# Kernel optimization log

Measured on AMD Instinct MI355X. Metric: run time of the kernel, lower is better.

Reference implementation:

```python
import jax, jax.numpy as jnp
import numpy as np

GCN_DIM = 512
POS_EMB_DIM = 64
K = 8
L = 128  # uttr_len
B = 16
PAIR_FEAT = 2 * GCN_DIM + POS_EMB_DIM


def _pair_indices(L, K):
    # Static (trace-time) construction of the windowed pair list, matching the
    # torch masked_select over the full L*L pair grid: row p = i*L + j keeps
    # pairs with |j - i| <= K, in the same row-major order.
    i = np.repeat(np.arange(L), L)
    j = np.tile(np.arange(L), L)
    rel = j - i
    mask = np.abs(rel) <= K
    return i[mask], j[mask], rel[mask]


def setup_inputs() -> dict:
    key = jax.random.key(0)
    k1, k2, k3, k4, k5, k6, k7 = jax.random.split(key, 7)
    h_emo = jax.random.normal(k1, (B, L, GCN_DIM), dtype=jnp.float32)
    h_cause = jax.random.normal(k2, (B, L, GCN_DIM), dtype=jnp.float32)
    # xavier_uniform for embedding table
    lim_e = np.sqrt(6.0 / (2 * K + 1 + POS_EMB_DIM))
    pos_emb = jax.random.uniform(k3, (2 * K + 1, POS_EMB_DIM), minval=-lim_e, maxval=lim_e, dtype=jnp.float32)
    lim1 = np.sqrt(1.0 / PAIR_FEAT)
    W1 = jax.random.uniform(k4, (PAIR_FEAT, PAIR_FEAT), minval=-lim1, maxval=lim1, dtype=jnp.float32)
    b1 = jax.random.uniform(k5, (PAIR_FEAT,), minval=-lim1, maxval=lim1, dtype=jnp.float32)
    W2 = jax.random.uniform(k6, (1, PAIR_FEAT), minval=-lim1, maxval=lim1, dtype=jnp.float32)
    b2 = jax.random.uniform(k7, (1,), minval=-lim1, maxval=lim1, dtype=jnp.float32)
    return {
        "uttr_output_h_emotion": h_emo,
        "uttr_output_h_cause": h_cause,
        "pos_emb": pos_emb,
        "W1": W1,
        "b1": b1,
        "W2": W2,
        "b2": b2,
    }


def reference(uttr_output_h_emotion, uttr_output_h_cause, pos_emb, W1, b1, W2, b2):
    emo_idx, cau_idx, rel_np = _pair_indices(L, K)  # static numpy, length n
    emo_idx_j = jnp.asarray(emo_idx)
    cau_idx_j = jnp.asarray(cau_idx)
    rel = jnp.asarray(rel_np)  # [n], values in [-K, K]

    # windowed pair gather: couples_h = [H_emo[i] ; H_cause[j]]  -> [B, n, 2*g]
    P = jnp.concatenate(
        [uttr_output_h_emotion[:, emo_idx_j, :], uttr_output_h_cause[:, cau_idx_j, :]],
        axis=2,
    )

    # relative-position embedding + Gaussian kernel smoothing (batch-invariant)
    rel_emb = pos_emb[rel + K]  # [n, pos_emb_dim]
    rel_f = rel.astype(jnp.float32)
    kernel = jnp.exp(-jnp.square(rel_f[:, None] - rel_f[None, :]))  # [n, n]
    smoothed = kernel @ rel_emb  # [n, pos_emb_dim]

    couples = jnp.concatenate(
        [P, jnp.broadcast_to(smoothed[None], (P.shape[0],) + smoothed.shape)], axis=2
    )  # [B, n, PAIR_FEAT]

    h = jax.nn.relu(jnp.einsum("bnf,gf->bng", couples, W1) + b1)
    pred = (jnp.einsum("bnf,of->bno", h, W2) + b2).squeeze(-1)  # [B, n]

    emo_cau_pos = jnp.stack([emo_idx_j + 1, cau_idx_j + 1], axis=1)  # [n, 2], int
    return pred, emo_cau_pos
```

## Files before the change

### kernel.cpp

```cpp
#include <hip/hip_runtime.h>

typedef unsigned short u16;
typedef unsigned int u32;
typedef __attribute__((ext_vector_type(4))) float f32x4;
typedef __attribute__((ext_vector_type(8))) __bf16 bf16x8;
typedef __attribute__((ext_vector_type(4))) u16 u16x4;
typedef __attribute__((ext_vector_type(8))) u16 u16x8;
typedef __attribute__((ext_vector_type(4))) float f32x4v;

#define LSEQ 128
#define KW 8
#define NP 2104
#define MTOT 33664
#define FDIM 1088
#define GPAD 1152

#define WS_W1P  0ul
#define WS_EMOB 2506752ul
#define WS_CAUB 4603904ul
#define WS_SB   6701056ul
#define WS_TOFF 6738048ul
#define WS_EC   6738560ul

__device__ __forceinline__ u16 f2bf(float x) {
  union { float f; u32 u; } v; v.f = x;
  u32 r = v.u + 0x7fffu + ((v.u >> 16) & 1u);
  return (u16)(r >> 16);
}

__device__ __forceinline__ float bf2f(u16 x) {
  union { u32 u; float f; } v; v.u = ((u32)x) << 16; return v.f;
}

__device__ __forceinline__ void load_lds16(const void* g, void* l) {
  __builtin_amdgcn_global_load_lds(
      (const __attribute__((address_space(1))) void*)g,
      (__attribute__((address_space(3))) void*)l, 16, 0, 0);
}

__global__ __launch_bounds__(256)
void setup_all(const float* __restrict__ emo, const float* __restrict__ cau,
               const float* __restrict__ pos_emb, const float* __restrict__ W1,
               const float* __restrict__ b1,
               u16* __restrict__ W1p, u16* __restrict__ emoB,
               u16* __restrict__ cauB, u16* __restrict__ Sb,
               int* __restrict__ tab_off, float* __restrict__ out_pos) {
  __shared__ float smL[17 * 64];
  const int bx = blockIdx.x;
  const int t = threadIdx.x;
  if (bx < 612) {
    int idx = bx * 256 + t;
    int g = idx / 136;
    int f = (idx - g * 136) * 8;
    u16x8 o;
    if (g < 1088) {
      f32x4v v0 = *(const f32x4v*)&W1[g * 1088 + f];
      f32x4v v1 = *(const f32x4v*)&W1[g * 1088 + f + 4];
      o[0] = f2bf(v0.x); o[1] = f2bf(v0.y); o[2] = f2bf(v0.z); o[3] = f2bf(v0.w);
      o[4] = f2bf(v1.x); o[5] = f2bf(v1.y); o[6] = f2bf(v1.z); o[7] = f2bf(v1.w);
    } else {
      o = (u16x8)0;
    }
    *(u16x8*)&W1p[(size_t)g * 1088 + f] = o;
  } else if (bx < 1636) {
    int idx = (bx - 612) * 256 + t;
    const float* src;
    u16* dst;
    if (idx < 131072) { src = emo + idx * 8; dst = emoB + idx * 8; }
    else { int k = idx - 131072; src = cau + k * 8; dst = cauB + k * 8; }
    f32x4v v0 = *(const f32x4v*)src;
    f32x4v v1 = *(const f32x4v*)(src + 4);
    u16x8 o;
    o[0] = f2bf(v0.x); o[1] = f2bf(v0.y); o[2] = f2bf(v0.z); o[3] = f2bf(v0.w);
    o[4] = f2bf(v1.x); o[5] = f2bf(v1.y); o[6] = f2bf(v1.z); o[7] = f2bf(v1.w);
    *(u16x8*)dst = o;
  } else if (bx == 1636) {
    if (t < LSEQ) {
      int i = t;
      int off = 0;
      for (int tt = 0; tt < i; ++tt) {
        int lo = tt - KW; if (lo < 0) lo = 0;
        int hi = tt + KW; if (hi > LSEQ - 1) hi = LSEQ - 1;
        off += hi - lo + 1;
      }
      tab_off[i] = off;
      int jlo = i - KW; if (jlo < 0) jlo = 0;
      int jhi = i + KW; if (jhi > LSEQ - 1) jhi = LSEQ - 1;
      for (int j = jlo; j <= jhi; ++j) {
        int p = off + (j - jlo);
        out_pos[2 * p]     = (float)(i + 1);
        out_pos[2 * p + 1] = (float)(j + 1);
      }
    }
  } else {
    for (int idx = t; idx < 17 * 64; idx += 256) {
      int r = idx >> 6, d = idx & 63;
      float acc = 0.f;
      for (int s = 0; s < 17; ++s) {
        float diff = (float)(r - s);
        int a = s - 8; if (a < 0) a = -a;
        float cnt = (float)(128 - a);
        acc += cnt * expf(-diff * diff) * pos_emb[s * 64 + d];
      }
      smL[idx] = acc;
    }
    __syncthreads();
    int idx2 = (bx - 1637) * 256 + t;
    if (idx2 < 17 * 1088) {
      int r = idx2 / 1088;
      int g = idx2 - r * 1088;
      float a = b1[g];
      const float* wr = &W1[(size_t)g * 1088 + 1024];
      const float* sr = &smL[r * 64];
#pragma unroll 8
      for (int d = 0; d < 64; ++d) a = fmaf(sr[d], wr[d], a);
      Sb[r * 1088 + g] = f2bf(a);
    }
  }
}

__global__ __launch_bounds__(256, 4)
void feat_gemm(const u16* __restrict__ emoB, const u16* __restrict__ cauB,
               const u16* __restrict__ W1p, float* __restrict__ EC) {
  __shared__ __align__(16) u16 As2[2][64 * 32];
  __shared__ __align__(16) u16 Bs2[2][128 * 32];

  const int tid = threadIdx.x;
  const int mblk = blockIdx.x;
  const int gbase = blockIdx.y * 128;

  const int lane = tid & 63;
  const int w = tid >> 6;
  const int lrow = lane & 15;
  const int lk = (lane >> 4) * 8;
  const int wm = (w >> 1) * 32;
  const int wn = (w & 1) * 64;

  const int row0 = tid >> 2;
  const int sub = (tid & 3) * 8;

  const u16* Asrc = (mblk < 32) ? emoB : cauB;
  const int arow = (mblk & 31) * 64;
  const int fsel = (mblk < 32) ? 0 : 512;

  const u16* aP = Asrc + (size_t)(arow + row0) * 512 + sub;
  const u16* bP = W1p + (size_t)(gbase + row0) * FDIM + fsel + sub;
  const u16* bQ = bP + 64u * FDIM;

#define FSTAGE(ks, bb)                                                     \
  do {                                                                     \
    const int _f = (ks) * 32;                                              \
    load_lds16(aP + _f, (char*)&As2[bb][0] + tid * 16);                    \
    load_lds16(bP + _f, (char*)&Bs2[bb][0] + tid * 16);                    \
    load_lds16(bQ + _f, (char*)&Bs2[bb][0] + 4096 + tid * 16);             \
  } while (0)

  f32x4 acc[2][4];
#pragma unroll
  for (int mi = 0; mi < 2; ++mi)
#pragma unroll
    for (int ni = 0; ni < 4; ++ni) acc[mi][ni] = (f32x4){0.f, 0.f, 0.f, 0.f};

  FSTAGE(0, 0);
  asm volatile("s_waitcnt vmcnt(0)");
  __builtin_amdgcn_s_barrier();
  __builtin_amdgcn_sched_barrier(0);

  int cur = 0;
#pragma unroll 2
  for (int ks = 0; ks < 16; ++ks) {
    if (ks < 15) FSTAGE(ks + 1, cur ^ 1);

    bf16x8 av[2], bv[4];
#pragma unroll
    for (int mi = 0; mi < 2; ++mi)
      av[mi] = *(const bf16x8*)&As2[cur][(wm + mi * 16 + lrow) * 32 + lk];
#pragma unroll
    for (int ni = 0; ni < 4; ++ni)
      bv[ni] = *(const bf16x8*)&Bs2[cur][(wn + ni * 16 + lrow) * 32 + lk];
#pragma unroll
    for (int mi = 0; mi < 2; ++mi)
#pragma unroll
      for (int ni = 0; ni < 4; ++ni)
        acc[mi][ni] = __builtin_amdgcn_mfma_f32_16x16x32_bf16(av[mi], bv[ni], acc[mi][ni], 0, 0, 0);

    asm volatile("s_waitcnt vmcnt(0)");
    __builtin_amdgcn_s_barrier();
    __builtin_amdgcn_sched_barrier(0);
    cur ^= 1;
  }
#undef FSTAGE

  const int rbase = mblk * 64 + wm + ((lane >> 4) << 2);
#pragma unroll
  for (int mi = 0; mi < 2; ++mi) {
#pragma unroll
    for (int ni = 0; ni < 4; ++ni) {
      const int ocol = gbase + wn + ni * 16 + lrow;
      float* dst = EC + (size_t)(rbase + mi * 16) * GPAD + ocol;
#pragma unroll
      for (int r2 = 0; r2 < 4; ++r2) dst[(size_t)r2 * GPAD] = acc[mi][ni][r2];
    }
  }
}

__global__ __launch_bounds__(256, 4)
void combine(const float* __restrict__ EC, const u16* __restrict__ Sb,
             const float* __restrict__ W2, const float* __restrict__ b2,
             const int* __restrict__ tab_off, float* __restrict__ pred) {
  __shared__ __align__(16) u16 Sl[17 * 1088];
  __shared__ float partA[2][17], partB[2][17];

  const int tid = threadIdx.x;
  const int bid = blockIdx.x;
  const int sb = (bid & 7) * 128 + (bid >> 3);

  {
    char* dst = (char*)&Sl[0];
    const char* src = (const char*)Sb;
#pragma unroll
    for (int it = 0; it < 9; ++it)
      load_lds16(src + it * 4096 + tid * 16, dst + it * 4096 + tid * 16);
    if (tid < 8)
      load_lds16(src + 36864 + tid * 16, dst + 36864 + tid * 16);
  }

  const int w = tid >> 6;
  const int lane = tid & 63;
  const int h = w >> 1;
  const int gh = w & 1;
  const int u = sb * 2 + h;
  const int b = u >> 7;
  const int i = u & 127;
  int jlo = i - KW; if (jlo < 0) jlo = 0;
  int jhi = i + KW; if (jhi > 127) jhi = 127;

  const float bias2 = b2[0];
  const float* Erow = EC + (size_t)(b * 128 + i) * GPAD;
  const float* Cbase = EC + (size_t)(2048 + b * 128) * GPAD;

  const int g0 = gh * 512 + lane * 4;
  const int g1 = g0 + 256;
  const f32x4v e0 = *(const f32x4v*)(Erow + g0);
  const f32x4v e1 = *(const f32x4v*)(Erow + g1);
  const f32x4v w20 = *(const f32x4v*)(W2 + g0);
  const f32x4v w21 = *(const f32x4v*)(W2 + g1);
  float eT = 0.f, w2T = 0.f;
  if (gh) { eT = Erow[1024 + lane]; w2T = W2[1024 + lane]; }

  __syncthreads();

  const float* Crow = Cbase + (size_t)jlo * GPAD;
  f32x4v c0 = *(const f32x4v*)(Crow + g0);
  f32x4v c1 = *(const f32x4v*)(Crow + g1);
  float cT = gh ? Crow[1024 + lane] : 0.f;

  for (int j = jlo; j <= jhi; ++j) {
    f32x4v n0 = c0, n1 = c1; float nT = cT;
    if (j < jhi) {
      const float* Nrow = Cbase + (size_t)(j + 1) * GPAD;
      n0 = *(const f32x4v*)(Nrow + g0);
      n1 = *(const f32x4v*)(Nrow + g1);
      if (gh) nT = Nrow[1024 + lane];
    }
    const int r = j - i + KW;
    const u16* srow = &Sl[r * 1088];
    u16x4 sa = *(const u16x4*)(srow + g0);
    u16x4 sc = *(const u16x4*)(srow + g1);

    float a = 0.f;
    a = fmaf(fmaxf(e0.x + c0.x + bf2f(sa.x), 0.f), w20.x, a);
    a = fmaf(fmaxf(e0.y + c0.y + bf2f(sa.y), 0.f), w20.y, a);
    a = fmaf(fmaxf(e0.z + c0.z + bf2f(sa.z), 0.f), w20.z, a);
    a = fmaf(fmaxf(e0.w + c0.w + bf2f(sa.w), 0.f), w20.w, a);
    a = fmaf(fmaxf(e1.x + c1.x + bf2f(sc.x), 0.f), w21.x, a);
    a = fmaf(fmaxf(e1.y + c1.y + bf2f(sc.y), 0.f), w21.y, a);
    a = fmaf(fmaxf(e1.z + c1.z + bf2f(sc.z), 0.f), w21.z, a);
    a = fmaf(fmaxf(e1.w + c1.w + bf2f(sc.w), 0.f), w21.w, a);
    if (gh) {
      float sT = bf2f(srow[1024 + lane]);
      a = fmaf(fmaxf(eT + cT + sT, 0.f), w2T, a);
    }

    a += __shfl_xor(a, 1);
    a += __shfl_xor(a, 2);
    a += __shfl_xor(a, 4);
    a += __shfl_xor(a, 8);
    a += __shfl_xor(a, 16);
    a += __shfl_xor(a, 32);
    if (lane == 0) {
      if (gh) partB[h][j - jlo] = a;
      else    partA[h][j - jlo] = a;
    }
    c0 = n0; c1 = n1; cT = nT;
  }
  __syncthreads();

  if (w < 2) {
    const int u2 = sb * 2 + w;
    const int bb = u2 >> 7;
    const int i2 = u2 & 127;
    int jl2 = i2 - KW; if (jl2 < 0) jl2 = 0;
    int jh2 = i2 + KW; if (jh2 > 127) jh2 = 127;
    const int cnt2 = jh2 - jl2 + 1;
    if (lane < cnt2) {
      const int q = bb * NP + tab_off[i2] + lane;
      pred[q] = partA[w][lane] + partB[w][lane] + bias2;
    }
  }
}

extern "C" void kernel_launch(void* const* d_in, const int* in_sizes, int n_in,
                              void* d_out, int out_size, void* d_ws, size_t ws_size,
                              hipStream_t stream) {
  const float* h_emo = (const float*)d_in[0];
  const float* h_cau = (const float*)d_in[1];
  const float* pos_emb = (const float*)d_in[2];
  const float* W1 = (const float*)d_in[3];
  const float* b1 = (const float*)d_in[4];
  const float* W2 = (const float*)d_in[5];
  const float* b2 = (const float*)d_in[6];

  char* ws = (char*)d_ws;
  u16* W1p = (u16*)(ws + WS_W1P);
  u16* emoB = (u16*)(ws + WS_EMOB);
  u16* cauB = (u16*)(ws + WS_CAUB);
  u16* Sb = (u16*)(ws + WS_SB);
  int* tab_off = (int*)(ws + WS_TOFF);
  float* EC = (float*)(ws + WS_EC);

  float* pred = (float*)d_out;
  float* out_pos = (float*)d_out + MTOT;

  setup_all<<<1710, 256, 0, stream>>>(h_emo, h_cau, pos_emb, W1, b1,
                                      W1p, emoB, cauB, Sb, tab_off, out_pos);
  feat_gemm<<<dim3(64, 9), 256, 0, stream>>>(emoB, cauB, W1p, EC);
  combine<<<1024, 256, 0, stream>>>(EC, Sb, W2, b2, tab_off, pred);
}
```

Baseline: 110.3 us.

## Move position-bias setup into GEMM launch and read bias table from global

The position-bias table and position-output blocks move out of the conversion kernel and become extra blocks of the GEMM launch, which now uses a 1D grid with those blocks appended after the 576 GEMM tiles. The combine kernel no longer stages the 37 KB bias table into LDS and reads it directly from global memory, which drops a barrier and frees LDS for higher occupancy. The risk is more global or L2 traffic in the combine inner loop. The aux blocks are also scheduled last in the GEMM grid, so they may add tail time.

```diff
diff --git a/kernel.cpp b/kernel.cpp
--- a/kernel.cpp
+++ b/kernel.cpp
@@ -39,13 +39,10 @@
 }
 
 __global__ __launch_bounds__(256)
-void setup_all(const float* __restrict__ emo, const float* __restrict__ cau,
-               const float* __restrict__ pos_emb, const float* __restrict__ W1,
-               const float* __restrict__ b1,
-               u16* __restrict__ W1p, u16* __restrict__ emoB,
-               u16* __restrict__ cauB, u16* __restrict__ Sb,
-               int* __restrict__ tab_off, float* __restrict__ out_pos) {
-  __shared__ float smL[17 * 64];
+void convert_all(const float* __restrict__ emo, const float* __restrict__ cau,
+                 const float* __restrict__ W1,
+                 u16* __restrict__ W1p, u16* __restrict__ emoB,
+                 u16* __restrict__ cauB) {
   const int bx = blockIdx.x;
   const int t = threadIdx.x;
   if (bx < 612) {
@@ -62,7 +59,7 @@
       o = (u16x8)0;
     }
     *(u16x8*)&W1p[(size_t)g * 1088 + f] = o;
-  } else if (bx < 1636) {
+  } else {
     int idx = (bx - 612) * 256 + t;
     const float* src;
     u16* dst;
@@ -74,60 +71,72 @@
     o[0] = f2bf(v0.x); o[1] = f2bf(v0.y); o[2] = f2bf(v0.z); o[3] = f2bf(v0.w);
     o[4] = f2bf(v1.x); o[5] = f2bf(v1.y); o[6] = f2bf(v1.z); o[7] = f2bf(v1.w);
     *(u16x8*)dst = o;
-  } else if (bx == 1636) {
-    if (t < LSEQ) {
-      int i = t;
-      int off = 0;
-      for (int tt = 0; tt < i; ++tt) {
-        int lo = tt - KW; if (lo < 0) lo = 0;
-        int hi = tt + KW; if (hi > LSEQ - 1) hi = LSEQ - 1;
-        off += hi - lo + 1;
-      }
-      tab_off[i] = off;
-      int jlo = i - KW; if (jlo < 0) jlo = 0;
-      int jhi = i + KW; if (jhi > LSEQ - 1) jhi = LSEQ - 1;
-      for (int j = jlo; j <= jhi; ++j) {
-        int p = off + (j - jlo);
-        out_pos[2 * p]     = (float)(i + 1);
-        out_pos[2 * p + 1] = (float)(j + 1);
-      }
-    }
-  } else {
-    for (int idx = t; idx < 17 * 64; idx += 256) {
-      int r = idx >> 6, d = idx & 63;
-      float acc = 0.f;
-      for (int s = 0; s < 17; ++s) {
-        float diff = (float)(r - s);
-        int a = s - 8; if (a < 0) a = -a;
-        float cnt = (float)(128 - a);
-        acc += cnt * expf(-diff * diff) * pos_emb[s * 64 + d];
-      }
-      smL[idx] = acc;
-    }
-    __syncthreads();
-    int idx2 = (bx - 1637) * 256 + t;
-    if (idx2 < 17 * 1088) {
-      int r = idx2 / 1088;
-      int g = idx2 - r * 1088;
-      float a = b1[g];
-      const float* wr = &W1[(size_t)g * 1088 + 1024];
-      const float* sr = &smL[r * 64];
-#pragma unroll 8
-      for (int d = 0; d < 64; ++d) a = fmaf(sr[d], wr[d], a);
-      Sb[r * 1088 + g] = f2bf(a);
-    }
   }
 }
 
 __global__ __launch_bounds__(256, 4)
-void feat_gemm(const u16* __restrict__ emoB, const u16* __restrict__ cauB,
-               const u16* __restrict__ W1p, float* __restrict__ EC) {
+void feat_aux(const u16* __restrict__ emoB, const u16* __restrict__ cauB,
+              const u16* __restrict__ W1p, float* __restrict__ EC,
+              const float* __restrict__ pos_emb, const float* __restrict__ W1,
+              const float* __restrict__ b1, u16* __restrict__ Sb,
+              int* __restrict__ tab_off, float* __restrict__ out_pos) {
   __shared__ __align__(16) u16 As2[2][64 * 32];
   __shared__ __align__(16) u16 Bs2[2][128 * 32];
 
+  const int bid = blockIdx.x;
   const int tid = threadIdx.x;
-  const int mblk = blockIdx.x;
-  const int gbase = blockIdx.y * 128;
+
+  if (bid >= 576) {
+    const int bid2 = bid - 576;
+    if (bid2 < 73) {
+      float* smL = (float*)&Bs2[0][0];
+      for (int idx = tid; idx < 17 * 64; idx += 256) {
+        int r = idx >> 6, d = idx & 63;
+        float acc = 0.f;
+        for (int s = 0; s < 17; ++s) {
+          float diff = (float)(r - s);
+          int a = s - 8; if (a < 0) a = -a;
+          float cnt = (float)(128 - a);
+          acc += cnt * expf(-diff * diff) * pos_emb[s * 64 + d];
+        }
+        smL[idx] = acc;
+      }
+      __syncthreads();
+      int idx2 = bid2 * 256 + tid;
+      if (idx2 < 17 * 1088) {
+        int r = idx2 / 1088;
+        int g = idx2 - r * 1088;
+        float a = b1[g];
+        const float* wr = &W1[(size_t)g * 1088 + 1024];
+        const float* sr = &smL[r * 64];
+#pragma unroll 8
+        for (int d = 0; d < 64; ++d) a = fmaf(sr[d], wr[d], a);
+        Sb[idx2] = f2bf(a);
+      }
+    } else {
+      if (tid < LSEQ) {
+        int i = tid;
+        int off = 0;
+        for (int tt = 0; tt < i; ++tt) {
+          int lo = tt - KW; if (lo < 0) lo = 0;
+          int hi = tt + KW; if (hi > LSEQ - 1) hi = LSEQ - 1;
+          off += hi - lo + 1;
+        }
+        tab_off[i] = off;
+        int jlo = i - KW; if (jlo < 0) jlo = 0;
+        int jhi = i + KW; if (jhi > LSEQ - 1) jhi = LSEQ - 1;
+        for (int j = jlo; j <= jhi; ++j) {
+          int p = off + (j - jlo);
+          out_pos[2 * p]     = (float)(i + 1);
+          out_pos[2 * p + 1] = (float)(j + 1);
+        }
+      }
+    }
+    return;
+  }
+
+  const int mblk = bid & 63;
+  const int gbase = (bid >> 6) * 128;
 
   const int lane = tid & 63;
   const int w = tid >> 6;
@@ -208,22 +217,11 @@
 void combine(const float* __restrict__ EC, const u16* __restrict__ Sb,
              const float* __restrict__ W2, const float* __restrict__ b2,
              const int* __restrict__ tab_off, float* __restrict__ pred) {
-  __shared__ __align__(16) u16 Sl[17 * 1088];
   __shared__ float partA[2][17], partB[2][17];
 
   const int tid = threadIdx.x;
   const int bid = blockIdx.x;
   const int sb = (bid & 7) * 128 + (bid >> 3);
-
-  {
-    char* dst = (char*)&Sl[0];
-    const char* src = (const char*)Sb;
-#pragma unroll
-    for (int it = 0; it < 9; ++it)
-      load_lds16(src + it * 4096 + tid * 16, dst + it * 4096 + tid * 16);
-    if (tid < 8)
-      load_lds16(src + 36864 + tid * 16, dst + 36864 + tid * 16);
-  }
 
   const int w = tid >> 6;
   const int lane = tid & 63;
@@ -248,8 +246,6 @@
   float eT = 0.f, w2T = 0.f;
   if (gh) { eT = Erow[1024 + lane]; w2T = W2[1024 + lane]; }
 
-  __syncthreads();
-
   const float* Crow = Cbase + (size_t)jlo * GPAD;
   f32x4v c0 = *(const f32x4v*)(Crow + g0);
   f32x4v c1 = *(const f32x4v*)(Crow + g1);
@@ -264,7 +260,7 @@
       if (gh) nT = Nrow[1024 + lane];
     }
     const int r = j - i + KW;
-    const u16* srow = &Sl[r * 1088];
+    const u16* srow = Sb + r * 1088;
     u16x4 sa = *(const u16x4*)(srow + g0);
     u16x4 sc = *(const u16x4*)(srow + g1);
 
@@ -332,8 +328,8 @@
   float* pred = (float*)d_out;
   float* out_pos = (float*)d_out + MTOT;
 
-  setup_all<<<1710, 256, 0, stream>>>(h_emo, h_cau, pos_emb, W1, b1,
-                                      W1p, emoB, cauB, Sb, tab_off, out_pos);
-  feat_gemm<<<dim3(64, 9), 256, 0, stream>>>(emoB, cauB, W1p, EC);
+  convert_all<<<1636, 256, 0, stream>>>(h_emo, h_cau, W1, W1p, emoB, cauB);
+  feat_aux<<<650, 256, 0, stream>>>(emoB, cauB, W1p, EC,
+                                    pos_emb, W1, b1, Sb, tab_off, out_pos);
   combine<<<1024, 256, 0, stream>>>(EC, Sb, W2, b2, tab_off, pred);
 }
```

New measurement: 108.7 us. No clear change (-1.4%).
